# Optimization experiments

Hardware: AMD Instinct MI355X
Metric: run time of the kernel (lower is better)

## Reference

```python
import jax, jax.numpy as jnp
import numpy as np

N, CT, C, L, H, W, HEAD, GROUPS = 4, 512, 512, 256, 64, 64, 16, 16


def setup_inputs() -> dict:
    key = jax.random.key(0)
    ks = jax.random.split(key, 8)
    d_in_g = C // GROUPS
    return {
        "feature": jax.random.normal(ks[0], (N, C, H, W), dtype=jnp.float32),
        "token": jax.random.normal(ks[1], (N, CT, L), dtype=jnp.float32),
        # conv1x1_1d value/key projections: weight [C_out, C_in]
        "Wv": jax.random.normal(ks[2], (C, CT), dtype=jnp.float32) * (1.0 / np.sqrt(CT)),
        "bv": jnp.zeros((C,), dtype=jnp.float32),
        "Wk": jax.random.normal(ks[3], (C, CT), dtype=jnp.float32) * (1.0 / np.sqrt(CT)),
        "bk": jnp.zeros((C,), dtype=jnp.float32),
        # grouped conv1x1_2d query projection: weight [groups, C_out/g, C_in/g]
        "Wq": jax.random.normal(ks[4], (GROUPS, d_in_g, d_in_g), dtype=jnp.float32) * (1.0 / np.sqrt(d_in_g)),
        "bq": jnp.zeros((C,), dtype=jnp.float32),
    }


def reference(feature, token, Wv, bv, Wk, bk, Wq, bq):
    h = HEAD
    d = C // h              # per-head dim
    S = H * W               # query positions
    # value / key: 1x1 conv1d == matmul over channel dim
    proj_v = (jnp.einsum('oc,ncl->nol', Wv, token) + bv[None, :, None]).reshape(N, h, d, L)
    proj_k = (jnp.einsum('oc,ncl->nol', Wk, token) + bk[None, :, None]).reshape(N, h, d, L)
    # query: grouped 1x1 conv2d (padding=0; see notes) == per-group matmul
    f_g = feature.reshape(N, GROUPS, C // GROUPS, S)
    q = jnp.einsum('goi,ngis->ngos', Wq, f_g).reshape(N, C, S) + bq[None, :, None]
    proj_q = q.reshape(N, h, d, S).transpose(0, 1, 3, 2)  # [N, h, S, d]
    scale = 1.0 / np.sqrt(C / h)
    scores = jnp.einsum('nhsd,nhdl->nhsl', proj_q, proj_k) * scale  # [N,h,S,L]
    proj_coef = jax.nn.softmax(scores, axis=3)
    proj = jnp.einsum('nhdl,nhsl->nhds', proj_v, proj_coef)  # [N,h,d,S]
    return feature + proj.reshape(N, C, H, W)
```

## Files before the change

kernel.cpp:

```cpp
#include <hip/hip_runtime.h>

typedef float f32x4 __attribute__((ext_vector_type(4)));
typedef short bf16x8 __attribute__((ext_vector_type(8)));
typedef __bf16 bf2 __attribute__((ext_vector_type(2)));
typedef unsigned short u16;
typedef unsigned int u32;

#define CT_ 512
#define C_ 512
#define L_ 256
#define S_ 4096
#define D_ 32

static __device__ __forceinline__ u16 f2bf(float x) {
    union { __bf16 h; u16 u; } v; v.h = (__bf16)x; return v.u;
}
static __device__ __forceinline__ u32 packbf(float a, float b) {
    union { bf2 h; u32 u; } v;
    v.h[0] = (__bf16)a; v.h[1] = (__bf16)b;
    return v.u;
}

__global__ __launch_bounds__(256) void prep_all(const float* __restrict__ Wv,
                                                const float* __restrict__ Wk,
                                                const float* __restrict__ token,
                                                u16* __restrict__ wbf,
                                                u16* __restrict__ tokT) {
    __shared__ float tile[32][33];
    int bx = blockIdx.x;
    int t = threadIdx.x;
    if (bx < 256) {
        int idx = (bx * 256 + t) * 8;
        const float* src = (idx < 262144) ? (Wv + idx) : (Wk + (idx - 262144));
        float4 a = *(const float4*)src;
        float4 b = *(const float4*)(src + 4);
        uint4 o;
        o.x = packbf(a.x, a.y);
        o.y = packbf(a.z, a.w);
        o.z = packbf(b.x, b.y);
        o.w = packbf(b.z, b.w);
        *(uint4*)(wbf + idx) = o;
    } else {
        int b2 = bx - 256;
        int ct_t = b2 & 15, l_t = (b2 >> 4) & 7, n = b2 >> 7;
        int r = t >> 3, c4 = (t & 7) * 4;
        const float* src = token + ((size_t)n * CT_ + ct_t * 32 + r) * L_ + l_t * 32 + c4;
        float4 v = *(const float4*)src;
        tile[r][c4] = v.x; tile[r][c4 + 1] = v.y; tile[r][c4 + 2] = v.z; tile[r][c4 + 3] = v.w;
        __syncthreads();
        uint2 o;
        o.x = packbf(tile[c4][r],     tile[c4 + 1][r]);
        o.y = packbf(tile[c4 + 2][r], tile[c4 + 3][r]);
        *(uint2*)(tokT + ((size_t)n * L_ + l_t * 32 + r) * CT_ + ct_t * 32 + c4) = o;
    }
}

__global__ __launch_bounds__(64) void kv_gemm(const u16* __restrict__ Wv_bf,
                                              const u16* __restrict__ Wk_bf,
                                              const u16* __restrict__ tokT,
                                              const float* __restrict__ bv,
                                              const float* __restrict__ bk,
                                              u16* __restrict__ V_ws,
                                              u16* __restrict__ KT_ws) {
    int bx = blockIdx.x;
    int l_t = bx & 7, c_t = (bx >> 3) & 15, kv = (bx >> 7) & 1, n = bx >> 8;
    const u16* W = kv ? Wk_bf : Wv_bf;
    const float* bias = kv ? bk : bv;
    int c0 = c_t * 32, l0 = l_t * 32;
    int lane = threadIdx.x;
    int lr = lane & 15, g = lane >> 4;

    const f32x4 fz = {0.f, 0.f, 0.f, 0.f};
    f32x4 acc[2][2] = {{fz, fz}, {fz, fz}};

    const u16* Abase = W + (size_t)(c0 + lr) * CT_ + g * 8;
    const u16* Bbase = tokT + ((size_t)n * L_ + l0 + lr) * CT_ + g * 8;

#pragma unroll
    for (int k = 0; k < 16; ++k) {
        bf16x8 a0 = *(const bf16x8*)(Abase + k * 32);
        bf16x8 a1 = *(const bf16x8*)(Abase + (size_t)16 * CT_ + k * 32);
        bf16x8 b0 = *(const bf16x8*)(Bbase + k * 32);
        bf16x8 b1 = *(const bf16x8*)(Bbase + (size_t)16 * CT_ + k * 32);
        acc[0][0] = __builtin_amdgcn_mfma_f32_16x16x32_bf16(a0, b0, acc[0][0], 0, 0, 0);
        acc[0][1] = __builtin_amdgcn_mfma_f32_16x16x32_bf16(a0, b1, acc[0][1], 0, 0, 0);
        acc[1][0] = __builtin_amdgcn_mfma_f32_16x16x32_bf16(a1, b0, acc[1][0], 0, 0, 0);
        acc[1][1] = __builtin_amdgcn_mfma_f32_16x16x32_bf16(a1, b1, acc[1][1], 0, 0, 0);
    }

    float bb[2][4];
#pragma unroll
    for (int i = 0; i < 2; ++i)
#pragma unroll
        for (int r = 0; r < 4; ++r) bb[i][r] = bias[c0 + i * 16 + g * 4 + r];

    if (kv == 0) {
#pragma unroll
        for (int i = 0; i < 2; ++i)
#pragma unroll
            for (int jt = 0; jt < 2; ++jt) {
                int l = l0 + jt * 16 + lr;
#pragma unroll
                for (int r = 0; r < 4; ++r) {
                    int c = c0 + i * 16 + g * 4 + r;
                    V_ws[((size_t)n * C_ + c) * L_ + l] = f2bf(acc[i][jt][r] + bb[i][r]);
                }
            }
    } else {
#pragma unroll
        for (int jt = 0; jt < 2; ++jt) {
            int l = l0 + jt * 16 + lr;
#pragma unroll
            for (int i = 0; i < 2; ++i) {
                uint2 o;
                o.x = packbf(acc[i][jt][0] + bb[i][0], acc[i][jt][1] + bb[i][1]);
                o.y = packbf(acc[i][jt][2] + bb[i][2], acc[i][jt][3] + bb[i][3]);
                *(uint2*)(KT_ws + ((size_t)n * L_ + l) * C_ + c0 + i * 16 + g * 4) = o;
            }
        }
    }
}

__global__ __launch_bounds__(256, 3) void attn(const float* __restrict__ feature,
                                               const float* __restrict__ Wq,
                                               const float* __restrict__ bq,
                                               const u16* __restrict__ V_ws,
                                               const u16* __restrict__ KT_ws,
                                               float* __restrict__ out) {
    __shared__ u16 KT_lds[256][40];
    __shared__ u16 V_lds[32][264];
    __shared__ u16 Q_lds[64][40];
    __shared__ u16 wq_lds[32][40];
    __shared__ float bq_lds[32];

    int bx = blockIdx.x;
    int sb = bx & 63, h = (bx >> 6) & 15, n = bx >> 10;
    int s0 = sb * 64;
    int t = threadIdx.x;
    int w = t >> 6, lane = t & 63, lr = lane & 15, g = lane >> 4;
    const f32x4 fz = {0.f, 0.f, 0.f, 0.f};

    {
        int lq = t & 63, cb = (t >> 6) * 8;
#pragma unroll
        for (int i = 0; i < 4; ++i) {
            int l = i * 64 + lq;
            uint4 v = *(const uint4*)(KT_ws + ((size_t)n * L_ + l) * C_ + h * D_ + cb);
            *(uint4*)&KT_lds[l][cb] = v;
        }
    }
    {
        int d = t & 31, cb32 = (t >> 5) * 32;
        const u16* src = V_ws + ((size_t)n * C_ + h * D_ + d) * L_ + cb32;
#pragma unroll
        for (int i = 0; i < 8; ++i) {
            int in4 = ((i & 1) << 2) | (i >> 1);
            uint2 v = *(const uint2*)(src + in4 * 4);
            *(uint2*)&V_lds[d][cb32 + i * 4] = v;
        }
    }
    {
        int r = t >> 3, c4 = (t & 7) * 4;
        float4 v = *(const float4*)(Wq + ((size_t)h * D_ + r) * D_ + c4);
        *(u32*)&wq_lds[r][c4]     = packbf(v.x, v.y);
        *(u32*)&wq_lds[r][c4 + 2] = packbf(v.z, v.w);
    }
    if (t < 32) bq_lds[t] = bq[h * D_ + t];
    __syncthreads();

    const float scale = 0.17677669529663687f * 1.4426950408889634f;
    {
        union { u16 u[8]; bf16x8 v; } au;
        const float* fbase = feature + ((size_t)n * C_ + h * D_) * S_ + s0 + w * 16 + lr;
#pragma unroll
        for (int j = 0; j < 8; ++j)
            au.u[j] = f2bf(fbase[(size_t)(g * 8 + j) * S_]);
#pragma unroll
        for (int dt = 0; dt < 2; ++dt) {
            bf16x8 b = *(const bf16x8*)&wq_lds[dt * 16 + lr][g * 8];
            f32x4 aq = __builtin_amdgcn_mfma_f32_16x16x32_bf16(au.v, b, fz, 0, 0, 0);
            int dout = dt * 16 + lr;
            float bqv = bq_lds[dout];
#pragma unroll
            for (int r = 0; r < 4; ++r)
                Q_lds[w * 16 + g * 4 + r][dout] = f2bf((aq[r] + bqv) * scale);
        }
    }

    f32x4 accs[16];
    {
        bf16x8 q = *(const bf16x8*)&Q_lds[w * 16 + lr][g * 8];
#pragma unroll
        for (int lt = 0; lt < 16; ++lt) {
            bf16x8 a = *(const bf16x8*)&KT_lds[lt * 16 + lr][g * 8];
            accs[lt] = __builtin_amdgcn_mfma_f32_16x16x32_bf16(a, q, fz, 0, 0, 0);
        }
    }

    float s4[4] = {0.f, 0.f, 0.f, 0.f};
#pragma unroll
    for (int lt = 0; lt < 16; ++lt) {
#pragma unroll
        for (int r = 0; r < 4; ++r) {
            float e = __builtin_amdgcn_exp2f(accs[lt][r]);
            accs[lt][r] = e;
            s4[r] += e;
        }
    }
    float sum = (s4[0] + s4[1]) + (s4[2] + s4[3]);
    sum += __shfl_xor(sum, 16, 64);
    sum += __shfl_xor(sum, 32, 64);
    float inv_own = __builtin_amdgcn_rcpf(sum);

    f32x4 acco[2] = {fz, fz};
#pragma unroll
    for (int tc = 0; tc < 8; ++tc) {
        union { u32 d[4]; bf16x8 v; } pa;
#pragma unroll
        for (int j = 0; j < 4; ++j)
            pa.d[j] = packbf(accs[2 * tc + (j >> 1)][(j & 1) * 2],
                             accs[2 * tc + (j >> 1)][(j & 1) * 2 + 1]);
#pragma unroll
        for (int dt = 0; dt < 2; ++dt) {
            bf16x8 vb = *(const bf16x8*)&V_lds[dt * 16 + lr][tc * 32 + g * 8];
            acco[dt] = __builtin_amdgcn_mfma_f32_16x16x32_bf16(pa.v, vb, acco[dt], 0, 0, 0);
        }
    }

    float inv4[4];
#pragma unroll
    for (int r = 0; r < 4; ++r)
        inv4[r] = __shfl(inv_own, (lane & 48) | (g * 4 + r), 64);
#pragma unroll
    for (int dt = 0; dt < 2; ++dt) {
        size_t off = ((size_t)n * C_ + h * D_ + dt * 16 + lr) * S_ + s0 + w * 16 + g * 4;
        float4 f = *(const float4*)(feature + off);
        float4 o;
        o.x = f.x + acco[dt][0] * inv4[0];
        o.y = f.y + acco[dt][1] * inv4[1];
        o.z = f.z + acco[dt][2] * inv4[2];
        o.w = f.w + acco[dt][3] * inv4[3];
        *(float4*)(out + off) = o;
    }
}

extern "C" void kernel_launch(void* const* d_in, const int* in_sizes, int n_in,
                              void* d_out, int out_size, void* d_ws, size_t ws_size,
                              hipStream_t stream) {
    const float* feature = (const float*)d_in[0];
    const float* token   = (const float*)d_in[1];
    const float* Wv      = (const float*)d_in[2];
    const float* bv      = (const float*)d_in[3];
    const float* Wk      = (const float*)d_in[4];
    const float* bk      = (const float*)d_in[5];
    const float* Wq      = (const float*)d_in[6];
    const float* bq      = (const float*)d_in[7];
    float* out = (float*)d_out;

    u16* ws16  = (u16*)d_ws;
    u16* Wv_bf = ws16;
    u16* Wk_bf = Wv_bf + 262144;
    u16* tokT  = Wk_bf + 262144;
    u16* V_ws  = tokT + 524288;
    u16* KT_ws = V_ws + 524288;

    prep_all<<<dim3(768), dim3(256), 0, stream>>>(Wv, Wk, token, Wv_bf, tokT);
    kv_gemm<<<dim3(1024), dim3(64), 0, stream>>>(Wv_bf, Wk_bf, tokT, bv, bk, V_ws, KT_ws);
    attn<<<dim3(4096), dim3(256), 0, stream>>>(feature, Wq, bq, V_ws, KT_ws, out);
}
```

Measured before the change: 50.04 us.

## Loop four query tiles per block to reuse K/V tiles and keep Q in registers

```diff
diff --git a/kernel.cpp b/kernel.cpp
--- a/kernel.cpp
+++ b/kernel.cpp
@@ -11,6 +11,7 @@
 #define L_ 256
 #define S_ 4096
 #define D_ 32
+#define TILES 4
 
 static __device__ __forceinline__ u16 f2bf(float x) {
     union { __bf16 h; u16 u; } v; v.h = (__bf16)x; return v.u;
@@ -115,13 +116,13 @@
                 uint2 o;
                 o.x = packbf(acc[i][jt][0] + bb[i][0], acc[i][jt][1] + bb[i][1]);
                 o.y = packbf(acc[i][jt][2] + bb[i][2], acc[i][jt][3] + bb[i][3]);
-                *(uint2*)(KT_ws + ((size_t)n * L_ + l) * C_ + c0 + i * 16 + g * 4) = o;
-            }
-        }
-    }
-}
-
-__global__ __launch_bounds__(256, 3) void attn(const float* __restrict__ feature,
+                *(uint2*)(KT_ws + ((size_t)n * L_ + l) * C_ + c0 + g * 8 + i * 4) = o;
+            }
+        }
+    }
+}
+
+__global__ __launch_bounds__(256, 4) void attn(const float* __restrict__ feature,
                                                const float* __restrict__ Wq,
                                                const float* __restrict__ bq,
                                                const u16* __restrict__ V_ws,
@@ -129,13 +130,10 @@
                                                float* __restrict__ out) {
     __shared__ u16 KT_lds[256][40];
     __shared__ u16 V_lds[32][264];
-    __shared__ u16 Q_lds[64][40];
-    __shared__ u16 wq_lds[32][40];
-    __shared__ float bq_lds[32];
 
     int bx = blockIdx.x;
-    int sb = bx & 63, h = (bx >> 6) & 15, n = bx >> 10;
-    int s0 = sb * 64;
+    int sg = bx & 15, h = (bx >> 4) & 15, n = bx >> 8;
+    int s_blk = sg * 256;
     int t = threadIdx.x;
     int w = t >> 6, lane = t & 63, lr = lane & 15, g = lane >> 4;
     const f32x4 fz = {0.f, 0.f, 0.f, 0.f};
@@ -159,88 +157,104 @@
             *(uint2*)&V_lds[d][cb32 + i * 4] = v;
         }
     }
-    {
-        int r = t >> 3, c4 = (t & 7) * 4;
-        float4 v = *(const float4*)(Wq + ((size_t)h * D_ + r) * D_ + c4);
-        *(u32*)&wq_lds[r][c4]     = packbf(v.x, v.y);
-        *(u32*)&wq_lds[r][c4 + 2] = packbf(v.z, v.w);
-    }
-    if (t < 32) bq_lds[t] = bq[h * D_ + t];
+
+    const float scale = 0.17677669529663687f * 1.4426950408889634f;
+    union { u32 d[4]; bf16x8 v; } wqf[2];
+#pragma unroll
+    for (int dt = 0; dt < 2; ++dt) {
+        const float* wsrc = Wq + ((size_t)h * D_ + dt * 16 + lr) * D_ + g * 8;
+        float4 w0 = *(const float4*)wsrc;
+        float4 w1 = *(const float4*)(wsrc + 4);
+        wqf[dt].d[0] = packbf(w0.x * scale, w0.y * scale);
+        wqf[dt].d[1] = packbf(w0.z * scale, w0.w * scale);
+        wqf[dt].d[2] = packbf(w1.x * scale, w1.y * scale);
+        wqf[dt].d[3] = packbf(w1.z * scale, w1.w * scale);
+    }
+    float bqs[2][4];
+#pragma unroll
+    for (int dt = 0; dt < 2; ++dt)
+#pragma unroll
+        for (int r = 0; r < 4; ++r)
+            bqs[dt][r] = bq[h * D_ + dt * 16 + g * 4 + r] * scale;
+
     __syncthreads();
 
-    const float scale = 0.17677669529663687f * 1.4426950408889634f;
-    {
-        union { u16 u[8]; bf16x8 v; } au;
-        const float* fbase = feature + ((size_t)n * C_ + h * D_) * S_ + s0 + w * 16 + lr;
-#pragma unroll
-        for (int j = 0; j < 8; ++j)
-            au.u[j] = f2bf(fbase[(size_t)(g * 8 + j) * S_]);
-#pragma unroll
-        for (int dt = 0; dt < 2; ++dt) {
-            bf16x8 b = *(const bf16x8*)&wq_lds[dt * 16 + lr][g * 8];
-            f32x4 aq = __builtin_amdgcn_mfma_f32_16x16x32_bf16(au.v, b, fz, 0, 0, 0);
-            int dout = dt * 16 + lr;
-            float bqv = bq_lds[dout];
-#pragma unroll
-            for (int r = 0; r < 4; ++r)
-                Q_lds[w * 16 + g * 4 + r][dout] = f2bf((aq[r] + bqv) * scale);
-        }
-    }
-
-    f32x4 accs[16];
-    {
-        bf16x8 q = *(const bf16x8*)&Q_lds[w * 16 + lr][g * 8];
+    const float* fb = feature + ((size_t)n * C_ + h * D_) * S_ + s_blk + w * 16 + lr;
+    float f[8];
+#pragma unroll
+    for (int j = 0; j < 8; ++j) f[j] = fb[(size_t)(g * 8 + j) * S_];
+
+    for (int tile = 0; tile < TILES; ++tile) {
+        union { u32 d[4]; bf16x8 v; } au;
+#pragma unroll
+        for (int k = 0; k < 4; ++k) au.d[k] = packbf(f[2 * k], f[2 * k + 1]);
+        if (tile + 1 < TILES) {
+#pragma unroll
+            for (int j = 0; j < 8; ++j)
+                f[j] = fb[(size_t)(g * 8 + j) * S_ + (tile + 1) * 64];
+        }
+
+        f32x4 aq0 = __builtin_amdgcn_mfma_f32_16x16x32_bf16(wqf[0].v, au.v, fz, 0, 0, 0);
+        f32x4 aq1 = __builtin_amdgcn_mfma_f32_16x16x32_bf16(wqf[1].v, au.v, fz, 0, 0, 0);
+        union { u32 d[4]; bf16x8 v; } qb;
+        qb.d[0] = packbf(aq0[0] + bqs[0][0], aq0[1] + bqs[0][1]);
+        qb.d[1] = packbf(aq0[2] + bqs[0][2], aq0[3] + bqs[0][3]);
+        qb.d[2] = packbf(aq1[0] + bqs[1][0], aq1[1] + bqs[1][1]);
+        qb.d[3] = packbf(aq1[2] + bqs[1][2], aq1[3] + bqs[1][3]);
+
+        f32x4 accs[16];
 #pragma unroll
         for (int lt = 0; lt < 16; ++lt) {
             bf16x8 a = *(const bf16x8*)&KT_lds[lt * 16 + lr][g * 8];
-            accs[lt] = __builtin_amdgcn_mfma_f32_16x16x32_bf16(a, q, fz, 0, 0, 0);
-        }
-    }
-
-    float s4[4] = {0.f, 0.f, 0.f, 0.f};
-#pragma unroll
-    for (int lt = 0; lt < 16; ++lt) {
-#pragma unroll
-        for (int r = 0; r < 4; ++r) {
-            float e = __builtin_amdgcn_exp2f(accs[lt][r]);
-            accs[lt][r] = e;
-            s4[r] += e;
-        }
-    }
-    float sum = (s4[0] + s4[1]) + (s4[2] + s4[3]);
-    sum += __shfl_xor(sum, 16, 64);
-    sum += __shfl_xor(sum, 32, 64);
-    float inv_own = __builtin_amdgcn_rcpf(sum);
-
-    f32x4 acco[2] = {fz, fz};
-#pragma unroll
-    for (int tc = 0; tc < 8; ++tc) {
-        union { u32 d[4]; bf16x8 v; } pa;
-#pragma unroll
-        for (int j = 0; j < 4; ++j)
-            pa.d[j] = packbf(accs[2 * tc + (j >> 1)][(j & 1) * 2],
-                             accs[2 * tc + (j >> 1)][(j & 1) * 2 + 1]);
+            accs[lt] = __builtin_amdgcn_mfma_f32_16x16x32_bf16(a, qb.v, fz, 0, 0, 0);
+        }
+
+        float s4[4] = {0.f, 0.f, 0.f, 0.f};
+#pragma unroll
+        for (int lt = 0; lt < 16; ++lt) {
+#pragma unroll
+            for (int r = 0; r < 4; ++r) {
+                float e = __builtin_amdgcn_exp2f(accs[lt][r]);
+                accs[lt][r] = e;
+                s4[r] += e;
+            }
+        }
+        float sum = (s4[0] + s4[1]) + (s4[2] + s4[3]);
+        sum += __shfl_xor(sum, 16, 64);
+        sum += __shfl_xor(sum, 32, 64);
+        float inv_own = __builtin_amdgcn_rcpf(sum);
+
+        f32x4 acco[2] = {fz, fz};
+#pragma unroll
+        for (int tc = 0; tc < 8; ++tc) {
+            union { u32 d[4]; bf16x8 v; } pa;
+#pragma unroll
+            for (int j = 0; j < 4; ++j)
+                pa.d[j] = packbf(accs[2 * tc + (j >> 1)][(j & 1) * 2],
+                                 accs[2 * tc + (j >> 1)][(j & 1) * 2 + 1]);
+#pragma unroll
+            for (int dt = 0; dt < 2; ++dt) {
+                bf16x8 vb = *(const bf16x8*)&V_lds[dt * 16 + lr][tc * 32 + g * 8];
+                acco[dt] = __builtin_amdgcn_mfma_f32_16x16x32_bf16(pa.v, vb, acco[dt], 0, 0, 0);
+            }
+        }
+
+        float inv4[4];
+#pragma unroll
+        for (int r = 0; r < 4; ++r)
+            inv4[r] = __shfl(inv_own, (lane & 48) | (g * 4 + r), 64);
 #pragma unroll
         for (int dt = 0; dt < 2; ++dt) {
-            bf16x8 vb = *(const bf16x8*)&V_lds[dt * 16 + lr][tc * 32 + g * 8];
-            acco[dt] = __builtin_amdgcn_mfma_f32_16x16x32_bf16(pa.v, vb, acco[dt], 0, 0, 0);
-        }
-    }
-
-    float inv4[4];
-#pragma unroll
-    for (int r = 0; r < 4; ++r)
-        inv4[r] = __shfl(inv_own, (lane & 48) | (g * 4 + r), 64);
-#pragma unroll
-    for (int dt = 0; dt < 2; ++dt) {
-        size_t off = ((size_t)n * C_ + h * D_ + dt * 16 + lr) * S_ + s0 + w * 16 + g * 4;
-        float4 f = *(const float4*)(feature + off);
-        float4 o;
-        o.x = f.x + acco[dt][0] * inv4[0];
-        o.y = f.y + acco[dt][1] * inv4[1];
-        o.z = f.z + acco[dt][2] * inv4[2];
-        o.w = f.w + acco[dt][3] * inv4[3];
-        *(float4*)(out + off) = o;
+            size_t off = ((size_t)n * C_ + h * D_ + dt * 16 + lr) * S_
+                       + s_blk + tile * 64 + w * 16 + g * 4;
+            float4 fe = *(const float4*)(feature + off);
+            float4 o;
+            o.x = fe.x + acco[dt][0] * inv4[0];
+            o.y = fe.y + acco[dt][1] * inv4[1];
+            o.z = fe.z + acco[dt][2] * inv4[2];
+            o.w = fe.w + acco[dt][3] * inv4[3];
+            *(float4*)(out + off) = o;
+        }
     }
 }
 
@@ -266,5 +280,5 @@
 
     prep_all<<<dim3(768), dim3(256), 0, stream>>>(Wv, Wk, token, Wv_bf, tokT);
     kv_gemm<<<dim3(1024), dim3(64), 0, stream>>>(Wv_bf, Wk_bf, tokT, bv, bk, V_ws, KT_ws);
-    attn<<<dim3(4096), dim3(256), 0, stream>>>(feature, Wq, bq, V_ws, KT_ws, out);
-}
+    attn<<<dim3(1024), dim3(256), 0, stream>>>(feature, Wq, bq, V_ws, KT_ws, out);
+}
```

Result: slower. 57.94 us (+15.8%).
